# Kernel tuning notes

Hardware: AMD Instinct MI355X
Metric: run time of the kernel (lower is better)

Reference implementation:

```python
import jax, jax.numpy as jnp
import numpy as np

N_NODES = 50000
N_EDGES = 1250000
D_NODE = 64
D_EDGE = 64
M_OUT = 64
U_OUT = 64


def setup_inputs() -> dict:
    key = jax.random.key(0)
    k1, k2, k3, k4, k5, k6 = jax.random.split(key, 6)
    H = jax.random.normal(k1, (N_NODES, D_NODE), dtype=jnp.float32)
    Xe = jax.random.normal(k2, (N_EDGES, D_EDGE), dtype=jnp.float32)
    id_Xe = jax.random.randint(k3, (2, N_EDGES), 0, N_NODES, dtype=jnp.int64)
    # Linear weights, torch convention: W @ x.T form, i.e. y = x @ W.T + b
    M_W = jax.random.normal(k4, (M_OUT, D_NODE + D_EDGE), dtype=jnp.float32) * 0.05
    M_b = jnp.zeros((M_OUT,), dtype=jnp.float32)
    U_W = jax.random.normal(k5, (U_OUT, D_NODE + M_OUT), dtype=jnp.float32) * 0.05
    U_b = jnp.zeros((U_OUT,), dtype=jnp.float32)
    return {"H": H, "Xe": Xe, "id_Xe": id_Xe, "M_W": M_W, "M_b": M_b, "U_W": U_W, "U_b": U_b}


def reference(H, Xe, id_Xe, M_W, M_b, U_b=None, U_W=None):
    # keep explicit signature matching setup_inputs keys
    pass


def reference(H, Xe, id_Xe, M_W, M_b, U_W, U_b):
    # gather source-node features: [E, d_node]
    features = H[id_Xe[0]]
    # message MLP: Linear + ReLU on [E, d_node + d_edge]
    M_in = jnp.concatenate([features, Xe], axis=1)
    Y = jax.nn.relu(M_in @ M_W.T + M_b)  # [E, M_OUT]
    # scatter-add (SUM aggregation) into destination nodes: [N, M_OUT]
    Z = jax.ops.segment_sum(Y, id_Xe[1], num_segments=H.shape[0])
    # update MLP: Linear + ReLU on [N, d_node + M_OUT]
    U_in = jnp.concatenate([H, Z], axis=1)
    H_next = jax.nn.relu(U_in @ U_W.T + U_b)  # [N, U_OUT]
    # dropout with p=0.0 is the identity
    return H_next
```

## Files before the change

kernel.cpp:

```cpp
#include <hip/hip_runtime.h>

typedef __attribute__((ext_vector_type(8))) short bf16x8;
typedef __attribute__((ext_vector_type(4))) float f32x4;

__device__ __forceinline__ unsigned short f2bf(float f) {
    union { float f; unsigned int u; } v; v.f = f;
    unsigned int r = v.u + 0x7FFFu + ((v.u >> 16) & 1u);
    return (unsigned short)(r >> 16);
}

__global__ __launch_bounds__(256)
void gnn_mlp(const float* __restrict__ A,
             const float* __restrict__ B2,
             const int* __restrict__ gidx,
             const int* __restrict__ sidx,
             const float* __restrict__ W,
             const float* __restrict__ bias,
             float* __restrict__ out,
             int rows, int ntiles)
{
    __shared__ char Ab[64 * 128 * 2];

    const int t    = threadIdx.x;
    const int wave = t >> 6;
    const int lane = t & 63;
    const int lrow = lane & 15;
    const int lko  = (lane >> 4) * 8;
    const int lko2 = lko * 2;

    bf16x8 bfrag[4][4];
#pragma unroll
    for (int f = 0; f < 4; ++f) {
#pragma unroll
        for (int ks = 0; ks < 4; ++ks) {
            const float* wp = W + (f * 16 + lrow) * 128 + ks * 32 + lko;
            bf16x8 v;
#pragma unroll
            for (int i = 0; i < 8; ++i)
                ((unsigned short*)&v)[i] = f2bf(wp[i]);
            bfrag[f][ks] = v;
        }
    }

    float bia[4];
#pragma unroll
    for (int f = 0; f < 4; ++f) bia[f] = bias[f * 16 + lrow];

    const int el = t >> 2;
    const int q  = t & 3;
    const int swz_w = (el & 7) << 4;

    for (int tile = blockIdx.x; tile < ntiles; tile += gridDim.x) {
        __syncthreads();
        {
            const long long e = (long long)tile * 64 + el;
            const bool ok = e < (long long)rows;
            long long arow = 0;
            if (ok) arow = gidx ? (long long)gidx[e] : e;
            const float* ap = A  + arow * 64;
            const float* bp = B2 + e * 64;
#pragma unroll
            for (int i = 0; i < 8; ++i) {
                const int c = q + 4 * i;
                float4 v = make_float4(0.f, 0.f, 0.f, 0.f);
                if (ok) v = (c < 16) ? *(const float4*)(ap + c * 4)
                                     : *(const float4*)(bp + (c - 16) * 4);
                unsigned int lo = (unsigned int)f2bf(v.x) | ((unsigned int)f2bf(v.y) << 16);
                unsigned int hi = (unsigned int)f2bf(v.z) | ((unsigned int)f2bf(v.w) << 16);
                *(uint2*)(Ab + ((el * 256 + c * 8) ^ swz_w)) = make_uint2(lo, hi);
            }
        }
        __syncthreads();

        f32x4 acc[4] = {{0.f,0.f,0.f,0.f},{0.f,0.f,0.f,0.f},
                        {0.f,0.f,0.f,0.f},{0.f,0.f,0.f,0.f}};
        const int arl   = wave * 16 + lrow;
        const int rbase = arl * 256;
        const int swz_r = (arl & 7) << 4;
#pragma unroll
        for (int ks = 0; ks < 4; ++ks) {
            bf16x8 a = *(const bf16x8*)(Ab + ((rbase + ks * 64 + lko2) ^ swz_r));
#pragma unroll
            for (int f = 0; f < 4; ++f)
                acc[f] = __builtin_amdgcn_mfma_f32_16x16x32_bf16(a, bfrag[f][ks], acc[f], 0, 0, 0);
        }

        const long long erow0 = (long long)tile * 64 + wave * 16 + (lane >> 4) * 4;
#pragma unroll
        for (int r = 0; r < 4; ++r) {
            const long long e = erow0 + r;
            if (e < (long long)rows) {
                if (sidx) {
                    const long long d = (long long)sidx[e] * 64;
#pragma unroll
                    for (int f = 0; f < 4; ++f)
                        atomicAdd(out + d + f * 16 + lrow,
                                  fmaxf(acc[f][r] + bia[f], 0.f));
                } else {
                    const long long o = e * 64;
#pragma unroll
                    for (int f = 0; f < 4; ++f)
                        out[o + f * 16 + lrow] = fmaxf(acc[f][r] + bia[f], 0.f);
                }
            }
        }
    }
}

extern "C" void kernel_launch(void* const* d_in, const int* in_sizes, int n_in,
                              void* d_out, int out_size, void* d_ws, size_t ws_size,
                              hipStream_t stream)
{
    const float* H   = (const float*)d_in[0];
    const float* Xe  = (const float*)d_in[1];
    const int*   idx = (const int*)d_in[2];
    const float* M_W = (const float*)d_in[3];
    const float* M_b = (const float*)d_in[4];
    const float* U_W = (const float*)d_in[5];
    const float* U_b = (const float*)d_in[6];
    float* Hn = (float*)d_out;
    float* Z  = (float*)d_ws;

    const int n_nodes = out_size / 64;
    const int n_edges = in_sizes[1] / 64;

    hipMemsetAsync(Z, 0, (size_t)n_nodes * 64 * sizeof(float), stream);

    const int etiles = (n_edges + 63) / 64;
    gnn_mlp<<<1024, 256, 0, stream>>>(H, Xe, idx, idx + n_edges,
                                      M_W, M_b, Z, n_edges, etiles);

    const int ntiles = (n_nodes + 63) / 64;
    gnn_mlp<<<ntiles, 256, 0, stream>>>(H, Z, nullptr, nullptr,
                                        U_W, U_b, Hn, n_nodes, ntiles);
}
```

Measured before the change: 350.5 us.

## Sort edges by destination and pre-reduce messages before atomic scatter

```diff
diff --git a/kernel.cpp b/kernel.cpp
--- a/kernel.cpp
+++ b/kernel.cpp
@@ -9,46 +9,169 @@
     return (unsigned short)(r >> 16);
 }
 
+__global__ void hist_k(const int* __restrict__ dst, unsigned* __restrict__ counts, int E) {
+    for (int i = blockIdx.x * blockDim.x + threadIdx.x; i < E; i += gridDim.x * blockDim.x)
+        atomicAdd(&counts[dst[i]], 1u);
+}
+
+__global__ __launch_bounds__(1024)
+void scan_k(const unsigned* __restrict__ counts, unsigned* __restrict__ cursor, int N) {
+    __shared__ unsigned part[1024];
+    const int t = threadIdx.x;
+    const int chunk = (N + 1023) >> 10;
+    const int lo = t * chunk, hi = min(lo + chunk, N);
+    unsigned s = 0;
+    for (int i = lo; i < hi; ++i) s += counts[i];
+    part[t] = s;
+    __syncthreads();
+    for (int off = 1; off < 1024; off <<= 1) {
+        unsigned v = (t >= off) ? part[t - off] : 0u;
+        __syncthreads();
+        part[t] += v;
+        __syncthreads();
+    }
+    unsigned run = t ? part[t - 1] : 0u;
+    for (int i = lo; i < hi; ++i) { cursor[i] = run; run += counts[i]; }
+}
+
+__global__ void scatter_k(const int* __restrict__ src, const int* __restrict__ dst,
+                          unsigned* __restrict__ cursor, unsigned* __restrict__ eord,
+                          int* __restrict__ esrc, int* __restrict__ edst, int E) {
+    for (int i = blockIdx.x * blockDim.x + threadIdx.x; i < E; i += gridDim.x * blockDim.x) {
+        int d = dst[i];
+        unsigned p = atomicAdd(&cursor[d], 1u);
+        eord[p] = (unsigned)i;
+        if (esrc) { esrc[p] = src[i]; edst[p] = d; }
+    }
+}
+
 __global__ __launch_bounds__(256)
-void gnn_mlp(const float* __restrict__ A,
-             const float* __restrict__ B2,
-             const int* __restrict__ gidx,
-             const int* __restrict__ sidx,
-             const float* __restrict__ W,
-             const float* __restrict__ bias,
-             float* __restrict__ out,
-             int rows, int ntiles)
+void edge_fused(const float* __restrict__ H, const float* __restrict__ Xe,
+                const int* __restrict__ src, const int* __restrict__ dst,
+                const unsigned* __restrict__ eord,
+                const int* __restrict__ esrc, const int* __restrict__ edst,
+                const float* __restrict__ W, const float* __restrict__ bias,
+                float* __restrict__ Z, int E, int ntiles)
+{
+    __shared__ float smem[64 * 68];
+    __shared__ int sdst[64];
+    char* Ab = reinterpret_cast<char*>(smem);
+
+    const int t = threadIdx.x, wave = t >> 6, lane = t & 63;
+    const int lrow = lane & 15, lko = (lane >> 4) * 8, lko2 = lko * 2;
+
+    bf16x8 wfrag[4][4];
+#pragma unroll
+    for (int f = 0; f < 4; ++f)
+#pragma unroll
+        for (int ks = 0; ks < 4; ++ks) {
+            const float* wp = W + (f * 16 + lrow) * 128 + ks * 32 + lko;
+            bf16x8 v;
+#pragma unroll
+            for (int i = 0; i < 8; ++i) ((unsigned short*)&v)[i] = f2bf(wp[i]);
+            wfrag[f][ks] = v;
+        }
+    const int fo = (lane >> 4) * 4;
+    f32x4 bia[4];
+#pragma unroll
+    for (int f = 0; f < 4; ++f) bia[f] = *(const f32x4*)(bias + f * 16 + fo);
+
+    const int el = t >> 2, q = t & 3, swz_w = (el & 7) << 4;
+
+    for (int tile = blockIdx.x; tile < ntiles; tile += gridDim.x) {
+        __syncthreads();
+        {
+            const long long p = (long long)tile * 64 + el;
+            const bool ok = p < (long long)E;
+            int e = 0, sv = 0;
+            if (ok) {
+                e  = (int)eord[p];
+                sv = esrc ? esrc[p] : src[e];
+            }
+            if (q == 0) sdst[el] = ok ? (edst ? edst[p] : dst[e]) : -1;
+            const float* ap = H  + (long long)sv * 64;
+            const float* bp = Xe + (long long)e * 64;
+#pragma unroll
+            for (int i = 0; i < 8; ++i) {
+                const int c = q + 4 * i;
+                float4 v = make_float4(0.f, 0.f, 0.f, 0.f);
+                if (ok) v = (c < 16) ? *(const float4*)(ap + c * 4)
+                                     : *(const float4*)(bp + (c - 16) * 4);
+                unsigned lo32 = (unsigned)f2bf(v.x) | ((unsigned)f2bf(v.y) << 16);
+                unsigned hi32 = (unsigned)f2bf(v.z) | ((unsigned)f2bf(v.w) << 16);
+                *(uint2*)(Ab + ((el * 256 + c * 8) ^ swz_w)) = make_uint2(lo32, hi32);
+            }
+        }
+        __syncthreads();
+
+        f32x4 acc[4] = {{0,0,0,0},{0,0,0,0},{0,0,0,0},{0,0,0,0}};
+        const int arl = wave * 16 + lrow, rbase = arl * 256, swz_r = (arl & 7) << 4;
+#pragma unroll
+        for (int ks = 0; ks < 4; ++ks) {
+            bf16x8 a = *(const bf16x8*)(Ab + ((rbase + ks * 64 + lko2) ^ swz_r));
+#pragma unroll
+            for (int f = 0; f < 4; ++f)
+                acc[f] = __builtin_amdgcn_mfma_f32_16x16x32_bf16(wfrag[f][ks], a, acc[f], 0, 0, 0);
+        }
+        __syncthreads();
+
+        {
+            const int erow = wave * 16 + (lane & 15);
+            float* yr = smem + erow * 68;
+#pragma unroll
+            for (int f = 0; f < 4; ++f) {
+                f32x4 y;
+#pragma unroll
+                for (int r = 0; r < 4; ++r) y[r] = fmaxf(acc[f][r] + bia[f][r], 0.f);
+                *(f32x4*)(yr + f * 16 + fo) = y;
+            }
+        }
+        __syncthreads();
+
+        {
+            const int f  = t & 63;
+            const int r0 = (t >> 6) * 16;
+            float a = 0.f;
+            int cur = sdst[r0];
+            for (int r = r0; r < r0 + 16; ++r) {
+                int d = sdst[r];
+                if (d != cur) {
+                    if (cur >= 0) atomicAdd(Z + (long long)cur * 64 + f, a);
+                    a = 0.f; cur = d;
+                }
+                a += smem[r * 68 + f];
+            }
+            if (cur >= 0) atomicAdd(Z + (long long)cur * 64 + f, a);
+        }
+    }
+}
+
+__global__ __launch_bounds__(256)
+void gnn_mlp(const float* __restrict__ A, const float* __restrict__ B2,
+             const int* __restrict__ gidx, const int* __restrict__ sidx,
+             const float* __restrict__ W, const float* __restrict__ bias,
+             float* __restrict__ out, int rows, int ntiles)
 {
     __shared__ char Ab[64 * 128 * 2];
-
-    const int t    = threadIdx.x;
-    const int wave = t >> 6;
-    const int lane = t & 63;
-    const int lrow = lane & 15;
-    const int lko  = (lane >> 4) * 8;
-    const int lko2 = lko * 2;
+    const int t = threadIdx.x, wave = t >> 6, lane = t & 63;
+    const int lrow = lane & 15, lko = (lane >> 4) * 8, lko2 = lko * 2;
 
     bf16x8 bfrag[4][4];
 #pragma unroll
-    for (int f = 0; f < 4; ++f) {
+    for (int f = 0; f < 4; ++f)
 #pragma unroll
         for (int ks = 0; ks < 4; ++ks) {
             const float* wp = W + (f * 16 + lrow) * 128 + ks * 32 + lko;
             bf16x8 v;
 #pragma unroll
-            for (int i = 0; i < 8; ++i)
-                ((unsigned short*)&v)[i] = f2bf(wp[i]);
+            for (int i = 0; i < 8; ++i) ((unsigned short*)&v)[i] = f2bf(wp[i]);
             bfrag[f][ks] = v;
         }
-    }
-
     float bia[4];
 #pragma unroll
     for (int f = 0; f < 4; ++f) bia[f] = bias[f * 16 + lrow];
 
-    const int el = t >> 2;
-    const int q  = t & 3;
-    const int swz_w = (el & 7) << 4;
+    const int el = t >> 2, q = t & 3, swz_w = (el & 7) << 4;
 
     for (int tile = blockIdx.x; tile < ntiles; tile += gridDim.x) {
         __syncthreads();
@@ -65,18 +188,15 @@
                 float4 v = make_float4(0.f, 0.f, 0.f, 0.f);
                 if (ok) v = (c < 16) ? *(const float4*)(ap + c * 4)
                                      : *(const float4*)(bp + (c - 16) * 4);
-                unsigned int lo = (unsigned int)f2bf(v.x) | ((unsigned int)f2bf(v.y) << 16);
-                unsigned int hi = (unsigned int)f2bf(v.z) | ((unsigned int)f2bf(v.w) << 16);
-                *(uint2*)(Ab + ((el * 256 + c * 8) ^ swz_w)) = make_uint2(lo, hi);
-            }
-        }
-        __syncthreads();
-
-        f32x4 acc[4] = {{0.f,0.f,0.f,0.f},{0.f,0.f,0.f,0.f},
-                        {0.f,0.f,0.f,0.f},{0.f,0.f,0.f,0.f}};
-        const int arl   = wave * 16 + lrow;
-        const int rbase = arl * 256;
-        const int swz_r = (arl & 7) << 4;
+                unsigned lo32 = (unsigned)f2bf(v.x) | ((unsigned)f2bf(v.y) << 16);
+                unsigned hi32 = (unsigned)f2bf(v.z) | ((unsigned)f2bf(v.w) << 16);
+                *(uint2*)(Ab + ((el * 256 + c * 8) ^ swz_w)) = make_uint2(lo32, hi32);
+            }
+        }
+        __syncthreads();
+
+        f32x4 acc[4] = {{0,0,0,0},{0,0,0,0},{0,0,0,0},{0,0,0,0}};
+        const int arl = wave * 16 + lrow, rbase = arl * 256, swz_r = (arl & 7) << 4;
 #pragma unroll
         for (int ks = 0; ks < 4; ++ks) {
             bf16x8 a = *(const bf16x8*)(Ab + ((rbase + ks * 64 + lko2) ^ swz_r));
@@ -94,8 +214,7 @@
                     const long long d = (long long)sidx[e] * 64;
 #pragma unroll
                     for (int f = 0; f < 4; ++f)
-                        atomicAdd(out + d + f * 16 + lrow,
-                                  fmaxf(acc[f][r] + bia[f], 0.f));
+                        atomicAdd(out + d + f * 16 + lrow, fmaxf(acc[f][r] + bia[f], 0.f));
                 } else {
                     const long long o = e * 64;
 #pragma unroll
@@ -119,18 +238,42 @@
     const float* U_W = (const float*)d_in[5];
     const float* U_b = (const float*)d_in[6];
     float* Hn = (float*)d_out;
-    float* Z  = (float*)d_ws;
 
     const int n_nodes = out_size / 64;
     const int n_edges = in_sizes[1] / 64;
+    const int* src = idx;
+    const int* dst = idx + n_edges;
+
+    char* ws = (char*)d_ws;
+    float* Z = (float*)ws;
+    size_t off = (size_t)n_nodes * 64 * sizeof(float);
+    unsigned* counts = (unsigned*)(ws + off); off += (size_t)n_nodes * 4;
+    unsigned* cursor = (unsigned*)(ws + off); off += (size_t)n_nodes * 4;
+    unsigned* eord   = (unsigned*)(ws + off); off += (size_t)n_edges * 4;
+    int* esrc = (int*)(ws + off); off += (size_t)n_edges * 4;
+    int* edst = (int*)(ws + off); off += (size_t)n_edges * 4;
+    const size_t need_full = off;
+    const size_t need_min  = need_full - 2ull * (size_t)n_edges * 4;
 
     hipMemsetAsync(Z, 0, (size_t)n_nodes * 64 * sizeof(float), stream);
 
     const int etiles = (n_edges + 63) / 64;
-    gnn_mlp<<<1024, 256, 0, stream>>>(H, Xe, idx, idx + n_edges,
-                                      M_W, M_b, Z, n_edges, etiles);
+    if (ws_size >= need_min) {
+        const bool full = ws_size >= need_full;
+        hipMemsetAsync(counts, 0, (size_t)n_nodes * 4, stream);
+        hist_k<<<1024, 256, 0, stream>>>(dst, counts, n_edges);
+        scan_k<<<1, 1024, 0, stream>>>(counts, cursor, n_nodes);
+        scatter_k<<<1024, 256, 0, stream>>>(src, dst, cursor, eord,
+                                            full ? esrc : nullptr,
+                                            full ? edst : nullptr, n_edges);
+        edge_fused<<<2048, 256, 0, stream>>>(H, Xe, src, dst, eord,
+                                             full ? esrc : nullptr,
+                                             full ? edst : nullptr,
+                                             M_W, M_b, Z, n_edges, etiles);
+    } else {
+        gnn_mlp<<<2048, 256, 0, stream>>>(H, Xe, src, dst, M_W, M_b, Z, n_edges, etiles);
+    }
 
     const int ntiles = (n_nodes + 63) / 64;
-    gnn_mlp<<<ntiles, 256, 0, stream>>>(H, Z, nullptr, nullptr,
-                                        U_W, U_b, Hn, n_nodes, ntiles);
-}
+    gnn_mlp<<<ntiles, 256, 0, stream>>>(H, Z, nullptr, nullptr, U_W, U_b, Hn, n_nodes, ntiles);
+}
```

Result: slower. 508.3 us (+45.0%).

## Precompute node-side message projection and scatter packed bf16 atomics

Applied to the files above, without the earlier changes.

```diff
diff --git a/kernel.cpp b/kernel.cpp
--- a/kernel.cpp
+++ b/kernel.cpp
@@ -9,74 +9,207 @@
     return (unsigned short)(r >> 16);
 }
 
+__device__ __forceinline__ void atomic_pk_bf16(unsigned short* p, float lo, float hi) {
+    unsigned v;
+    asm("v_cvt_pk_bf16_f32 %0, %1, %2" : "=v"(v) : "v"(lo), "v"(hi));
+    asm volatile("global_atomic_pk_add_bf16 %0, %1, off" :: "v"(p), "v"(v) : "memory");
+}
+
+__global__ void zero_k(unsigned* __restrict__ p, long long nw) {
+    long long i = ((long long)blockIdx.x * blockDim.x + threadIdx.x) * 4;
+    const long long st = (long long)gridDim.x * blockDim.x * 4;
+    for (; i + 4 <= nw; i += st) *(uint4*)(p + i) = make_uint4(0, 0, 0, 0);
+    for (; i < nw; ++i) p[i] = 0u;
+}
+
 __global__ __launch_bounds__(256)
-void gnn_mlp(const float* __restrict__ A,
-             const float* __restrict__ B2,
-             const int* __restrict__ gidx,
-             const int* __restrict__ sidx,
-             const float* __restrict__ W,
-             const float* __restrict__ bias,
-             float* __restrict__ out,
-             int rows, int ntiles)
+void gemm_g(const float* __restrict__ H, const float* __restrict__ MW,
+            const float* __restrict__ Mb, float* __restrict__ G, int rows)
+{
+    __shared__ char Ab[64 * 128];
+    const int t = threadIdx.x, wave = t >> 6, lane = t & 63;
+    const int lrow = lane & 15, kc = lane >> 4, lko = kc * 8, fo = kc * 4;
+
+    bf16x8 wfrag[4][2];
+#pragma unroll
+    for (int f = 0; f < 4; ++f)
+#pragma unroll
+        for (int ks = 0; ks < 2; ++ks) {
+            const float* wp = MW + (f * 16 + lrow) * 128 + ks * 32 + lko;
+            bf16x8 v;
+#pragma unroll
+            for (int i = 0; i < 8; ++i) ((unsigned short*)&v)[i] = f2bf(wp[i]);
+            wfrag[f][ks] = v;
+        }
+    f32x4 bia[4];
+#pragma unroll
+    for (int f = 0; f < 4; ++f) bia[f] = *(const f32x4*)(Mb + f * 16 + fo);
+
+    const int el = t >> 2, q = t & 3;
+    const int tiles = (rows + 63) >> 6;
+    for (int tile = blockIdx.x; tile < tiles; tile += gridDim.x) {
+        __syncthreads();
+        {
+            const long long e = (long long)tile * 64 + el;
+            const bool ok = e < (long long)rows;
+            const float* ap = H + e * 64;
+#pragma unroll
+            for (int i = 0; i < 4; ++i) {
+                const int c = q * 4 + i;
+                float4 v = make_float4(0.f, 0.f, 0.f, 0.f);
+                if (ok) v = *(const float4*)(ap + c * 4);
+                unsigned lo32 = (unsigned)f2bf(v.x) | ((unsigned)f2bf(v.y) << 16);
+                unsigned hi32 = (unsigned)f2bf(v.z) | ((unsigned)f2bf(v.w) << 16);
+                *(uint2*)(Ab + el * 128 + ((c * 8) ^ ((el & 7) << 4))) = make_uint2(lo32, hi32);
+            }
+        }
+        __syncthreads();
+
+        f32x4 acc[4] = {{0,0,0,0},{0,0,0,0},{0,0,0,0},{0,0,0,0}};
+        const int drow = wave * 16 + lrow;
+#pragma unroll
+        for (int ks = 0; ks < 2; ++ks) {
+            bf16x8 a = *(const bf16x8*)(Ab + drow * 128 + ((ks * 64 + kc * 16) ^ ((drow & 7) << 4)));
+#pragma unroll
+            for (int f = 0; f < 4; ++f)
+                acc[f] = __builtin_amdgcn_mfma_f32_16x16x32_bf16(wfrag[f][ks], a, acc[f], 0, 0, 0);
+        }
+
+        const long long e = (long long)tile * 64 + wave * 16 + lrow;
+        if (e < (long long)rows) {
+            float* gp = G + e * 64 + fo;
+#pragma unroll
+            for (int f = 0; f < 4; ++f)
+                *(f32x4*)(gp + f * 16) = acc[f] + bia[f];
+        }
+    }
+}
+
+__global__ __launch_bounds__(256)
+void edge_atomic(const float* __restrict__ Xe,
+                 const int* __restrict__ src, const int* __restrict__ dst,
+                 const float* __restrict__ MW, const float* __restrict__ G,
+                 unsigned short* __restrict__ Zb, int E)
+{
+    __shared__ char Ab[64 * 128];
+    const int t = threadIdx.x, wave = t >> 6, lane = t & 63;
+    const int lrow = lane & 15, kc = lane >> 4, lko = kc * 8, fo = kc * 4;
+
+    bf16x8 wfrag[4][2];
+#pragma unroll
+    for (int f = 0; f < 4; ++f)
+#pragma unroll
+        for (int ks = 0; ks < 2; ++ks) {
+            const float* wp = MW + (f * 16 + lrow) * 128 + 64 + ks * 32 + lko;
+            bf16x8 v;
+#pragma unroll
+            for (int i = 0; i < 8; ++i) ((unsigned short*)&v)[i] = f2bf(wp[i]);
+            wfrag[f][ks] = v;
+        }
+
+    const int el = t >> 2, q = t & 3;
+    const int tiles = (E + 63) >> 6;
+    for (int tile = blockIdx.x; tile < tiles; tile += gridDim.x) {
+        __syncthreads();
+        {
+            const long long e = (long long)tile * 64 + el;
+            const bool ok = e < (long long)E;
+            const float* ap = Xe + e * 64;
+#pragma unroll
+            for (int i = 0; i < 4; ++i) {
+                const int c = q * 4 + i;
+                float4 v = make_float4(0.f, 0.f, 0.f, 0.f);
+                if (ok) v = *(const float4*)(ap + c * 4);
+                unsigned lo32 = (unsigned)f2bf(v.x) | ((unsigned)f2bf(v.y) << 16);
+                unsigned hi32 = (unsigned)f2bf(v.z) | ((unsigned)f2bf(v.w) << 16);
+                *(uint2*)(Ab + el * 128 + ((c * 8) ^ ((el & 7) << 4))) = make_uint2(lo32, hi32);
+            }
+        }
+        __syncthreads();
+
+        f32x4 acc[4] = {{0,0,0,0},{0,0,0,0},{0,0,0,0},{0,0,0,0}};
+        const int drow = wave * 16 + lrow;
+#pragma unroll
+        for (int ks = 0; ks < 2; ++ks) {
+            bf16x8 a = *(const bf16x8*)(Ab + drow * 128 + ((ks * 64 + kc * 16) ^ ((drow & 7) << 4)));
+#pragma unroll
+            for (int f = 0; f < 4; ++f)
+                acc[f] = __builtin_amdgcn_mfma_f32_16x16x32_bf16(wfrag[f][ks], a, acc[f], 0, 0, 0);
+        }
+
+        const long long e = (long long)tile * 64 + wave * 16 + lrow;
+        if (e < (long long)E) {
+            const int s = src[e];
+            const int d = dst[e];
+            const float* gp = G + (long long)s * 64 + fo;
+            unsigned short* zp = Zb + (long long)d * 64 + fo;
+#pragma unroll
+            for (int f = 0; f < 4; ++f) {
+                const f32x4 gv = *(const f32x4*)(gp + f * 16);
+                const float y0 = fmaxf(acc[f][0] + gv[0], 0.f);
+                const float y1 = fmaxf(acc[f][1] + gv[1], 0.f);
+                const float y2 = fmaxf(acc[f][2] + gv[2], 0.f);
+                const float y3 = fmaxf(acc[f][3] + gv[3], 0.f);
+                atomic_pk_bf16(zp + f * 16 + 0, y0, y1);
+                atomic_pk_bf16(zp + f * 16 + 2, y2, y3);
+            }
+        }
+    }
+}
+
+__global__ __launch_bounds__(256)
+void node_mlp(const float* __restrict__ H, const unsigned short* __restrict__ Zb,
+              const float* __restrict__ W, const float* __restrict__ bias,
+              float* __restrict__ out, int rows)
 {
     __shared__ char Ab[64 * 128 * 2];
-
-    const int t    = threadIdx.x;
-    const int wave = t >> 6;
-    const int lane = t & 63;
-    const int lrow = lane & 15;
-    const int lko  = (lane >> 4) * 8;
-    const int lko2 = lko * 2;
+    const int t = threadIdx.x, wave = t >> 6, lane = t & 63;
+    const int lrow = lane & 15, lko = (lane >> 4) * 8, lko2 = lko * 2;
 
     bf16x8 bfrag[4][4];
 #pragma unroll
-    for (int f = 0; f < 4; ++f) {
+    for (int f = 0; f < 4; ++f)
 #pragma unroll
         for (int ks = 0; ks < 4; ++ks) {
             const float* wp = W + (f * 16 + lrow) * 128 + ks * 32 + lko;
             bf16x8 v;
 #pragma unroll
-            for (int i = 0; i < 8; ++i)
-                ((unsigned short*)&v)[i] = f2bf(wp[i]);
+            for (int i = 0; i < 8; ++i) ((unsigned short*)&v)[i] = f2bf(wp[i]);
             bfrag[f][ks] = v;
         }
-    }
-
     float bia[4];
 #pragma unroll
     for (int f = 0; f < 4; ++f) bia[f] = bias[f * 16 + lrow];
 
-    const int el = t >> 2;
-    const int q  = t & 3;
-    const int swz_w = (el & 7) << 4;
-
-    for (int tile = blockIdx.x; tile < ntiles; tile += gridDim.x) {
+    const int el = t >> 2, q = t & 3, swz_w = (el & 7) << 4;
+    const int tiles = (rows + 63) >> 6;
+    for (int tile = blockIdx.x; tile < tiles; tile += gridDim.x) {
         __syncthreads();
         {
             const long long e = (long long)tile * 64 + el;
             const bool ok = e < (long long)rows;
-            long long arow = 0;
-            if (ok) arow = gidx ? (long long)gidx[e] : e;
-            const float* ap = A  + arow * 64;
-            const float* bp = B2 + e * 64;
+            const float* ap = H + e * 64;
+            const unsigned short* zp = Zb + e * 64;
 #pragma unroll
             for (int i = 0; i < 8; ++i) {
                 const int c = q + 4 * i;
-                float4 v = make_float4(0.f, 0.f, 0.f, 0.f);
-                if (ok) v = (c < 16) ? *(const float4*)(ap + c * 4)
-                                     : *(const float4*)(bp + (c - 16) * 4);
-                unsigned int lo = (unsigned int)f2bf(v.x) | ((unsigned int)f2bf(v.y) << 16);
-                unsigned int hi = (unsigned int)f2bf(v.z) | ((unsigned int)f2bf(v.w) << 16);
-                *(uint2*)(Ab + ((el * 256 + c * 8) ^ swz_w)) = make_uint2(lo, hi);
-            }
-        }
-        __syncthreads();
-
-        f32x4 acc[4] = {{0.f,0.f,0.f,0.f},{0.f,0.f,0.f,0.f},
-                        {0.f,0.f,0.f,0.f},{0.f,0.f,0.f,0.f}};
-        const int arl   = wave * 16 + lrow;
-        const int rbase = arl * 256;
-        const int swz_r = (arl & 7) << 4;
+                uint2 w2 = make_uint2(0u, 0u);
+                if (ok) {
+                    if (c < 16) {
+                        float4 v = *(const float4*)(ap + c * 4);
+                        w2.x = (unsigned)f2bf(v.x) | ((unsigned)f2bf(v.y) << 16);
+                        w2.y = (unsigned)f2bf(v.z) | ((unsigned)f2bf(v.w) << 16);
+                    } else {
+                        w2 = *(const uint2*)(zp + (c - 16) * 4);
+                    }
+                }
+                *(uint2*)(Ab + ((el * 256 + c * 8) ^ swz_w)) = w2;
+            }
+        }
+        __syncthreads();
+
+        f32x4 acc[4] = {{0,0,0,0},{0,0,0,0},{0,0,0,0},{0,0,0,0}};
+        const int arl = wave * 16 + lrow, rbase = arl * 256, swz_r = (arl & 7) << 4;
 #pragma unroll
         for (int ks = 0; ks < 4; ++ks) {
             bf16x8 a = *(const bf16x8*)(Ab + ((rbase + ks * 64 + lko2) ^ swz_r));
@@ -90,18 +223,10 @@
         for (int r = 0; r < 4; ++r) {
             const long long e = erow0 + r;
             if (e < (long long)rows) {
-                if (sidx) {
-                    const long long d = (long long)sidx[e] * 64;
-#pragma unroll
-                    for (int f = 0; f < 4; ++f)
-                        atomicAdd(out + d + f * 16 + lrow,
-                                  fmaxf(acc[f][r] + bia[f], 0.f));
-                } else {
-                    const long long o = e * 64;
-#pragma unroll
-                    for (int f = 0; f < 4; ++f)
-                        out[o + f * 16 + lrow] = fmaxf(acc[f][r] + bia[f], 0.f);
-                }
+                const long long o = e * 64;
+#pragma unroll
+                for (int f = 0; f < 4; ++f)
+                    out[o + f * 16 + lrow] = fmaxf(acc[f][r] + bia[f], 0.f);
             }
         }
     }
@@ -119,18 +244,22 @@
     const float* U_W = (const float*)d_in[5];
     const float* U_b = (const float*)d_in[6];
     float* Hn = (float*)d_out;
-    float* Z  = (float*)d_ws;
 
     const int n_nodes = out_size / 64;
     const int n_edges = in_sizes[1] / 64;
-
-    hipMemsetAsync(Z, 0, (size_t)n_nodes * 64 * sizeof(float), stream);
-
-    const int etiles = (n_edges + 63) / 64;
-    gnn_mlp<<<1024, 256, 0, stream>>>(H, Xe, idx, idx + n_edges,
-                                      M_W, M_b, Z, n_edges, etiles);
+    const int* src = idx;
+    const int* dst = idx + n_edges;
+
+    char* ws = (char*)d_ws;
+    float* G = (float*)ws;
+    unsigned short* Zb = (unsigned short*)(ws + (size_t)n_nodes * 64 * 4);
+
+    zero_k<<<1024, 256, 0, stream>>>((unsigned*)Zb, (long long)n_nodes * 32);
 
     const int ntiles = (n_nodes + 63) / 64;
-    gnn_mlp<<<ntiles, 256, 0, stream>>>(H, Z, nullptr, nullptr,
-                                        U_W, U_b, Hn, n_nodes, ntiles);
-}
+    gemm_g<<<ntiles, 256, 0, stream>>>(H, M_W, M_b, G, n_nodes);
+
+    edge_atomic<<<2048, 256, 0, stream>>>(Xe, src, dst, M_W, G, Zb, n_edges);
+
+    node_mlp<<<ntiles, 256, 0, stream>>>(H, Zb, U_W, U_b, Hn, n_nodes);
+}
```

New measurement: 570.0 us. 62.6% more time.
